# Kernel tuning notes

Hardware: AMD Instinct MI355X
Metric: run time of the kernel (lower is better)

## Reference

```python
import jax, jax.numpy as jnp
import numpy as np

NEG = -1.0e4  # log-semiring additive identity (Semiring.zero)


def setup_inputs() -> dict:
    key = jax.random.key(0)
    k1, k2 = jax.random.split(key)
    B, L, T = 32, 512, 64
    logits = jax.random.normal(k1, (B, L, T), dtype=jnp.float32)
    mask = jnp.ones((B, L), dtype=bool)
    # xavier_normal init for [T, T]: std = sqrt(2 / (T + T)) = 1/sqrt(T)
    transitions = jax.random.normal(k2, (T, T), dtype=jnp.float32) * (1.0 / np.sqrt(T))
    return {"logits": logits, "mask": mask, "transitions": transitions}


def _crf_log_partition(logits, mask, transitions):
    B, L, T = logits.shape
    maskf = mask.astype(logits.dtype)
    logits = logits * maskf[..., None]                       # zero masked positions
    m = maskf[:, 1:, None, None]                             # [B, L-1, 1, 1]
    trans = transitions[None, None] * m                      # [B, L-1, T, T]
    # potentials[b, t, i, j] = logits[b, t+1, j] + transitions[i, j]
    potentials = logits[:, 1:, None, :] + trans
    # masked steps are replaced by the log-semiring identity matrix
    eye = jnp.where(jnp.eye(T, dtype=bool), 0.0, NEG).astype(logits.dtype)
    potentials = potentials * m + eye * (1.0 - m)            # [B, L-1, T, T]

    start = logits[:, 0]                                     # [B, T]

    def step(alpha, P):
        # alpha: [B, T] (log-space), P: [B, T, T]
        # alpha'[j] = logsumexp_i alpha[i] + P[i, j]
        return jax.nn.logsumexp(alpha[:, :, None] + P, axis=1), None

    Pseq = jnp.moveaxis(potentials, 1, 0)                    # [L-1, B, T, T]
    alpha, _ = jax.lax.scan(step, start, Pseq)
    return jax.nn.logsumexp(alpha, axis=-1)                  # [B]


def reference(logits, mask, transitions):
    return _crf_log_partition(logits, mask, transitions)
```

## Files before the change

kernel.cpp:

```cpp
#include <hip/hip_runtime.h>
#include <hip/hip_bf16.h>


#define LL 512
#define TT 64
#define CHUNKS 8
#define SS (LL / CHUNKS)

typedef __attribute__((ext_vector_type(4))) short short4v;
typedef __attribute__((ext_vector_type(8))) short short8v;
typedef __attribute__((ext_vector_type(2))) unsigned int uint2v;
typedef __attribute__((ext_vector_type(4))) unsigned int uint4v;
typedef __attribute__((ext_vector_type(4))) float float4v;
typedef __attribute__((ext_vector_type(8))) __bf16 bf16x8;

__device__ __forceinline__ float4v mfma32(bf16x8 a, bf16x8 b, float4v c) {
#if defined(__HIP_DEVICE_COMPILE__)
    return __builtin_amdgcn_mfma_f32_16x16x32_bf16(a, b, c, 0, 0, 0);
#else
    return c;
#endif
}
__device__ __forceinline__ float rdlane_f(float v, int lane) {
    return __int_as_float(__builtin_amdgcn_readlane(__float_as_int(v), lane));
}
__device__ __forceinline__ float rdfirst_f(float v) {
    return __int_as_float(__builtin_amdgcn_readfirstlane(__float_as_int(v)));
}
__device__ __forceinline__ float bf2f(unsigned short u) {
    return __uint_as_float(((unsigned int)u) << 16);
}
__device__ __forceinline__ short f2bf(float f) {
    __hip_bfloat16 h = __float2bfloat16(f);
    return *reinterpret_cast<short*>(&h);
}
__device__ __forceinline__ unsigned int pack2bf(float a, float b) {
#if defined(__HIP_DEVICE_COMPILE__)
#if __has_builtin(__builtin_amdgcn_cvt_pk_bf16_f32)
    typedef __attribute__((ext_vector_type(2))) __bf16 bf16x2;
    bf16x2 r = __builtin_amdgcn_cvt_pk_bf16_f32(a, b);
    return __builtin_bit_cast(unsigned int, r);
#else
    return __builtin_amdgcn_perm(__float_as_uint(b) + 0x8000u,
                                 __float_as_uint(a) + 0x8000u,
                                 0x07060302u);
#endif
#else
    return 0u;
#endif
}
__device__ __forceinline__ bf16x8 packpair(const float4v& a, const float4v& b) {
    uint4v u;
    u[0] = pack2bf(a[0], a[1]);
    u[1] = pack2bf(a[2], a[3]);
    u[2] = pack2bf(b[0], b[1]);
    u[3] = pack2bf(b[2], b[3]);
    return __builtin_bit_cast(bf16x8, u);
}

__global__ __launch_bounds__(64, 1) void crf_chunk(
    const float* __restrict__ logits,
    const float* __restrict__ trans,
    unsigned short* __restrict__ Mws,
    float* __restrict__ lsws)
{
    __shared__ float sh_g[2][TT];
    const int L = threadIdx.x;
    const int c = L & 15;
    const int q = L >> 4;
    const int bid = blockIdx.x;
    const int w  = bid & 3;
    const int cc = (bid >> 2) & (CHUNKS - 1);
    const int b  = bid >> 5;

    bf16x8 Af8[4][2];
#pragma unroll
    for (int jt = 0; jt < 4; ++jt) {
#pragma unroll
        for (int kp = 0; kp < 2; ++kp) {
            short8v v;
#pragma unroll
            for (int e = 0; e < 8; ++e) {
                const int k = kp * 32 + 4 * q + (e & 3) + ((e >> 2) << 4);
                const int m = jt * 16 + c;
                v[e] = f2bf(__expf(trans[k * TT + m]));
            }
            Af8[jt][kp] = __builtin_bit_cast(bf16x8, v);
        }
    }

    const int rg = w * 16 + c;
    bf16x8 Nf8[2];
#pragma unroll
    for (int kp = 0; kp < 2; ++kp) {
        short8v v;
#pragma unroll
        for (int e = 0; e < 8; ++e) {
            const int k = kp * 32 + 4 * q + (e & 3) + ((e >> 2) << 4);
            v[e] = f2bf((k == rg) ? 1.0f : 0.0f);
        }
        Nf8[kp] = __builtin_bit_cast(bf16x8, v);
    }

    float ls = 0.0f;
    const float* lgb = logits + (size_t)b * (LL * TT);
    const int tb = (cc == 0) ? 1 : cc * SS;
    const int te = cc * SS + SS;

    float n1 = lgb[(tb + 1) * TT + L];
    float n2 = lgb[(tb + 2) * TT + L];
    float n3 = lgb[(tb + 3) * TT + L];
    sh_g[tb & 1][L] = __expf(lgb[tb * TT + L]);

    for (int t = tb; t < te; ++t) {
        float4v gx[4];
#pragma unroll
        for (int jt = 0; jt < 4; ++jt)
            gx[jt] = *reinterpret_cast<const float4v*>(&sh_g[t & 1][jt * 16 + 4 * q]);

        sh_g[(t + 1) & 1][L] = __expf(n1);
        n1 = n2; n2 = n3;
        const int tn = (t + 4 < LL) ? (t + 4) : (LL - 1);
        n3 = lgb[tn * TT + L];

        float4v y[4];
#pragma unroll
        for (int jt = 0; jt < 4; ++jt) {
            float4v a = {0.f, 0.f, 0.f, 0.f};
            a = mfma32(Af8[jt][0], Nf8[0], a);
            a = mfma32(Af8[jt][1], Nf8[1], a);
            y[jt] = a;
        }

#pragma unroll
        for (int jt = 0; jt < 4; ++jt) y[jt] = y[jt] * gx[jt];

        if ((t & 7) == 7) {
            float mx = 0.0f;
#pragma unroll
            for (int jt = 0; jt < 4; ++jt)
                mx = fmaxf(mx, fmaxf(fmaxf(y[jt][0], y[jt][1]), fmaxf(y[jt][2], y[jt][3])));
            mx = fmaxf(mx, __shfl_xor(mx, 16));
            mx = fmaxf(mx, __shfl_xor(mx, 32));
            const float sc = __builtin_amdgcn_rcpf(mx);
            ls += __logf(mx);
#pragma unroll
            for (int jt = 0; jt < 4; ++jt) y[jt] = y[jt] * sc;
        }

        Nf8[0] = packpair(y[0], y[1]);
        Nf8[1] = packpair(y[2], y[3]);
    }

    unsigned short* mp = Mws + ((size_t)(b * CHUNKS + cc) * TT + rg) * TT;
#pragma unroll
    for (int kp = 0; kp < 2; ++kp) {
        const uint4v u = __builtin_bit_cast(uint4v, Nf8[kp]);
        uint2v lo; lo[0] = u[0]; lo[1] = u[1];
        uint2v hi; hi[0] = u[2]; hi[1] = u[3];
        *reinterpret_cast<uint2v*>(mp + kp * 32 + 4 * q) = lo;
        *reinterpret_cast<uint2v*>(mp + kp * 32 + 16 + 4 * q) = hi;
    }
    if (q == 0) lsws[(b * CHUNKS + cc) * TT + rg] = ls;
}

__device__ __forceinline__ void loadch(const unsigned short* __restrict__ Mws,
                                       const float* __restrict__ lsws,
                                       int idx, int j, short8v (&buf)[8], float& lsv) {
    const short8v* row = reinterpret_cast<const short8v*>(Mws + ((size_t)idx * TT + j) * TT);
#pragma unroll
    for (int rb = 0; rb < 8; ++rb) buf[rb] = row[rb];
    lsv = lsws[idx * TT + j];
}

__device__ __forceinline__ float foldch(float A, float lsv, const short8v (&buf)[8]) {
    const float tv = A + lsv;
    const float K = rdfirst_f(tv);
    const float wv = __expf(tv - K);
    float s0 = 0.f, s1 = 0.f, s2 = 0.f, s3 = 0.f;
#pragma unroll
    for (int rb = 0; rb < 8; ++rb) {
        s0 = fmaf(rdlane_f(wv, rb * 8 + 0), bf2f((unsigned short)buf[rb][0]), s0);
        s1 = fmaf(rdlane_f(wv, rb * 8 + 1), bf2f((unsigned short)buf[rb][1]), s1);
        s2 = fmaf(rdlane_f(wv, rb * 8 + 2), bf2f((unsigned short)buf[rb][2]), s2);
        s3 = fmaf(rdlane_f(wv, rb * 8 + 3), bf2f((unsigned short)buf[rb][3]), s3);
        s0 = fmaf(rdlane_f(wv, rb * 8 + 4), bf2f((unsigned short)buf[rb][4]), s0);
        s1 = fmaf(rdlane_f(wv, rb * 8 + 5), bf2f((unsigned short)buf[rb][5]), s1);
        s2 = fmaf(rdlane_f(wv, rb * 8 + 6), bf2f((unsigned short)buf[rb][6]), s2);
        s3 = fmaf(rdlane_f(wv, rb * 8 + 7), bf2f((unsigned short)buf[rb][7]), s3);
    }
    return K + __logf((s0 + s1) + (s2 + s3));
}

__global__ __launch_bounds__(64, 1) void crf_combine(
    const float* __restrict__ logits,
    const unsigned short* __restrict__ Mws,
    const float* __restrict__ lsws,
    float* __restrict__ out)
{
    const int b = blockIdx.x;
    const int j = threadIdx.x;
    const int bch = b * CHUNKS;

    short8v bA[8], bB[8];
    float lsA, lsB;
    loadch(Mws, lsws, bch + 0, j, bA, lsA);

    float A = logits[(size_t)b * (LL * TT) + j];

#pragma unroll
    for (int p = 0; p < CHUNKS / 2; ++p) {
        loadch(Mws, lsws, bch + 2 * p + 1, j, bB, lsB);
        A = foldch(A, lsA, bA);
        if (2 * p + 2 < CHUNKS) loadch(Mws, lsws, bch + 2 * p + 2, j, bA, lsA);
        A = foldch(A, lsB, bB);
    }

    float K = A;
#pragma unroll
    for (int off = 32; off; off >>= 1) K = fmaxf(K, __shfl_xor(K, off));
    float e = __expf(A - K);
#pragma unroll
    for (int off = 32; off; off >>= 1) e += __shfl_xor(e, off);
    if (j == 0) out[b] = K + __logf(e);
}

extern "C" void kernel_launch(void* const* d_in, const int* in_sizes, int n_in,
                              void* d_out, int out_size, void* d_ws, size_t ws_size,
                              hipStream_t stream) {
    const float* logits = (const float*)d_in[0];
    const float* trans  = (const float*)d_in[2];
    float* out = (float*)d_out;

    const int B = in_sizes[1] / LL;

    unsigned short* Mws = (unsigned short*)d_ws;
    float* lsws = (float*)((char*)d_ws + (size_t)B * CHUNKS * TT * TT * sizeof(unsigned short));

    crf_chunk<<<dim3(B * CHUNKS * 4), dim3(64), 0, stream>>>(logits, trans, Mws, lsws);
    crf_combine<<<dim3(B), dim3(64), 0, stream>>>(logits, Mws, lsws, out);
}
```

Baseline: 84.22 us.

## Double chunk count and fold chunk matrices with MFMA in combine kernel

The sequence is split into 16 chunks instead of 8, halving the serial per-chunk recurrence length and doubling the number of chunk blocks. The combine kernel's per-chunk vector-matrix fold, previously 64 readlane-broadcast FMAs per lane, now stages the weights through shared memory, packs them to bf16 and runs them through 16x16x32 MFMAs. This trades more chunk matrices to fold and workspace traffic for a shorter critical path. The weight vector is also rounded to bf16, which adds rounding error, and the shared-memory staging has no explicit barrier, relying on the block being a single wavefront.

```diff
diff --git a/kernel.cpp b/kernel.cpp
--- a/kernel.cpp
+++ b/kernel.cpp
@@ -4,7 +4,7 @@
 
 #define LL 512
 #define TT 64
-#define CHUNKS 8
+#define CHUNKS 16
 #define SS (LL / CHUNKS)
 
 typedef __attribute__((ext_vector_type(4))) short short4v;
@@ -21,14 +21,8 @@
     return c;
 #endif
 }
-__device__ __forceinline__ float rdlane_f(float v, int lane) {
-    return __int_as_float(__builtin_amdgcn_readlane(__float_as_int(v), lane));
-}
 __device__ __forceinline__ float rdfirst_f(float v) {
     return __int_as_float(__builtin_amdgcn_readfirstlane(__float_as_int(v)));
-}
-__device__ __forceinline__ float bf2f(unsigned short u) {
-    return __uint_as_float(((unsigned int)u) << 16);
 }
 __device__ __forceinline__ short f2bf(float f) {
     __hip_bfloat16 h = __float2bfloat16(f);
@@ -71,7 +65,7 @@
     const int bid = blockIdx.x;
     const int w  = bid & 3;
     const int cc = (bid >> 2) & (CHUNKS - 1);
-    const int b  = bid >> 5;
+    const int b  = bid >> 6;
 
     bf16x8 Af8[4][2];
 #pragma unroll
@@ -164,32 +158,61 @@
     if (q == 0) lsws[(b * CHUNKS + cc) * TT + rg] = ls;
 }
 
-__device__ __forceinline__ void loadch(const unsigned short* __restrict__ Mws,
-                                       const float* __restrict__ lsws,
-                                       int idx, int j, short8v (&buf)[8], float& lsv) {
-    const short8v* row = reinterpret_cast<const short8v*>(Mws + ((size_t)idx * TT + j) * TT);
-#pragma unroll
-    for (int rb = 0; rb < 8; ++rb) buf[rb] = row[rb];
-    lsv = lsws[idx * TT + j];
-}
-
-__device__ __forceinline__ float foldch(float A, float lsv, const short8v (&buf)[8]) {
+
+__device__ __forceinline__ void loadB(const unsigned short* __restrict__ Mws,
+                                      const float* __restrict__ lsws,
+                                      int idx, int c, int q, int L,
+                                      bf16x8 (&Bf)[4][2], float& lsv) {
+    const unsigned short* mb = Mws + (size_t)idx * (TT * TT);
+#pragma unroll
+    for (int nt = 0; nt < 4; ++nt) {
+        const unsigned short* rp = mb + (nt * 16 + c) * TT;
+#pragma unroll
+        for (int kp = 0; kp < 2; ++kp) {
+            const short4v lo = *reinterpret_cast<const short4v*>(rp + 4 * q + 32 * kp);
+            const short4v hi = *reinterpret_cast<const short4v*>(rp + 4 * q + 32 * kp + 16);
+            short8v v;
+            v[0] = lo[0]; v[1] = lo[1]; v[2] = lo[2]; v[3] = lo[3];
+            v[4] = hi[0]; v[5] = hi[1]; v[6] = hi[2]; v[7] = hi[3];
+            Bf[nt][kp] = __builtin_bit_cast(bf16x8, v);
+        }
+    }
+    lsv = lsws[idx * TT + L];
+}
+
+__device__ __forceinline__ float foldm(float A, float lsv, const bf16x8 (&Bf)[4][2],
+                                       float* __restrict__ sh_tv, int c, int q, int L) {
     const float tv = A + lsv;
     const float K = rdfirst_f(tv);
-    const float wv = __expf(tv - K);
-    float s0 = 0.f, s1 = 0.f, s2 = 0.f, s3 = 0.f;
-#pragma unroll
-    for (int rb = 0; rb < 8; ++rb) {
-        s0 = fmaf(rdlane_f(wv, rb * 8 + 0), bf2f((unsigned short)buf[rb][0]), s0);
-        s1 = fmaf(rdlane_f(wv, rb * 8 + 1), bf2f((unsigned short)buf[rb][1]), s1);
-        s2 = fmaf(rdlane_f(wv, rb * 8 + 2), bf2f((unsigned short)buf[rb][2]), s2);
-        s3 = fmaf(rdlane_f(wv, rb * 8 + 3), bf2f((unsigned short)buf[rb][3]), s3);
-        s0 = fmaf(rdlane_f(wv, rb * 8 + 4), bf2f((unsigned short)buf[rb][4]), s0);
-        s1 = fmaf(rdlane_f(wv, rb * 8 + 5), bf2f((unsigned short)buf[rb][5]), s1);
-        s2 = fmaf(rdlane_f(wv, rb * 8 + 6), bf2f((unsigned short)buf[rb][6]), s2);
-        s3 = fmaf(rdlane_f(wv, rb * 8 + 7), bf2f((unsigned short)buf[rb][7]), s3);
-    }
-    return K + __logf((s0 + s1) + (s2 + s3));
+    sh_tv[L] = tv;
+    const float4v r0 = *reinterpret_cast<const float4v*>(&sh_tv[4 * q]);
+    const float4v r1 = *reinterpret_cast<const float4v*>(&sh_tv[4 * q + 16]);
+    const float4v r2 = *reinterpret_cast<const float4v*>(&sh_tv[4 * q + 32]);
+    const float4v r3 = *reinterpret_cast<const float4v*>(&sh_tv[4 * q + 48]);
+    float w0[4], w1[4], w2[4], w3[4];
+#pragma unroll
+    for (int e = 0; e < 4; ++e) {
+        w0[e] = __expf(r0[e] - K);
+        w1[e] = __expf(r1[e] - K);
+        w2[e] = __expf(r2[e] - K);
+        w3[e] = __expf(r3[e] - K);
+    }
+    uint4v ua, ub;
+    ua[0] = pack2bf(w0[0], w0[1]); ua[1] = pack2bf(w0[2], w0[3]);
+    ua[2] = pack2bf(w1[0], w1[1]); ua[3] = pack2bf(w1[2], w1[3]);
+    ub[0] = pack2bf(w2[0], w2[1]); ub[1] = pack2bf(w2[2], w2[3]);
+    ub[2] = pack2bf(w3[0], w3[1]); ub[3] = pack2bf(w3[2], w3[3]);
+    const bf16x8 A0 = __builtin_bit_cast(bf16x8, ua);
+    const bf16x8 A1 = __builtin_bit_cast(bf16x8, ub);
+
+    float4v a0 = {0.f, 0.f, 0.f, 0.f}, a1 = a0, a2 = a0, a3 = a0;
+    a0 = mfma32(A0, Bf[0][0], a0); a0 = mfma32(A1, Bf[0][1], a0);
+    a1 = mfma32(A0, Bf[1][0], a1); a1 = mfma32(A1, Bf[1][1], a1);
+    a2 = mfma32(A0, Bf[2][0], a2); a2 = mfma32(A1, Bf[2][1], a2);
+    a3 = mfma32(A0, Bf[3][0], a3); a3 = mfma32(A1, Bf[3][1], a3);
+
+    const float s = (q == 0) ? a0[0] : (q == 1) ? a1[0] : (q == 2) ? a2[0] : a3[0];
+    return K + __logf(s);
 }
 
 __global__ __launch_bounds__(64, 1) void crf_combine(
@@ -198,22 +221,25 @@
     const float* __restrict__ lsws,
     float* __restrict__ out)
 {
+    __shared__ float sh_tv[TT];
     const int b = blockIdx.x;
-    const int j = threadIdx.x;
+    const int L = threadIdx.x;
+    const int c = L & 15;
+    const int q = L >> 4;
     const int bch = b * CHUNKS;
 
-    short8v bA[8], bB[8];
+    bf16x8 BA[4][2], BB[4][2];
     float lsA, lsB;
-    loadch(Mws, lsws, bch + 0, j, bA, lsA);
-
-    float A = logits[(size_t)b * (LL * TT) + j];
+    loadB(Mws, lsws, bch + 0, c, q, L, BA, lsA);
+
+    float A = logits[(size_t)b * (LL * TT) + L];
 
 #pragma unroll
     for (int p = 0; p < CHUNKS / 2; ++p) {
-        loadch(Mws, lsws, bch + 2 * p + 1, j, bB, lsB);
-        A = foldch(A, lsA, bA);
-        if (2 * p + 2 < CHUNKS) loadch(Mws, lsws, bch + 2 * p + 2, j, bA, lsA);
-        A = foldch(A, lsB, bB);
+        loadB(Mws, lsws, bch + 2 * p + 1, c, q, L, BB, lsB);
+        A = foldm(A, lsA, BA, sh_tv, c, q, L);
+        if (2 * p + 2 < CHUNKS) loadB(Mws, lsws, bch + 2 * p + 2, c, q, L, BA, lsA);
+        A = foldm(A, lsB, BB, sh_tv, c, q, L);
     }
 
     float K = A;
@@ -222,7 +248,7 @@
     float e = __expf(A - K);
 #pragma unroll
     for (int off = 32; off; off >>= 1) e += __shfl_xor(e, off);
-    if (j == 0) out[b] = K + __logf(e);
+    if (L == 0) out[b] = K + __logf(e);
 }
 
 extern "C" void kernel_launch(void* const* d_in, const int* in_sizes, int n_in,
```

Result: slower. 88.73 us (+5.4%).
